# Kernel tuning notes

Measured on AMD Instinct MI355X. Metric: run time of the kernel, lower is better.

## Reference

```python
import jax, jax.numpy as jnp
import numpy as np


def _layernorm(x, g, b, eps=1e-5):
    m = x.mean(-1, keepdims=True)
    v = ((x - m) ** 2).mean(-1, keepdims=True)
    return (x - m) * jax.lax.rsqrt(v + eps) * g + b


def _silu(x):
    return x * jax.nn.sigmoid(x)


def _mamba_mixer(x, in_w, conv_w, conv_b, xp_w, dt_w, dt_b, A_log, Dp, out_w):
    # x: (B, L, C) ; HF Mamba slow-path math
    B, L, C = x.shape
    dI = in_w.shape[0] // 2
    h, gate = jnp.split(x @ in_w.T, 2, axis=-1)  # (B, L, dI) each
    hc = jnp.transpose(h, (0, 2, 1))             # (B, dI, L)
    K = conv_w.shape[-1]
    hc = jax.lax.conv_general_dilated(hc, conv_w, (1,), [(K - 1, 0)],
                                      feature_group_count=dI,
                                      dimension_numbers=('NCH', 'OIH', 'NCH'))
    hc = _silu(hc + conv_b[None, :, None])
    u = jnp.transpose(hc, (0, 2, 1))             # (B, L, dI)
    R = dt_w.shape[1]
    N = A_log.shape[1]
    dt, Bs, Cs = jnp.split(u @ xp_w.T, [R, R + N], axis=-1)
    dt = jax.nn.softplus(dt @ dt_w.T + dt_b)     # (B, L, dI)
    A = -jnp.exp(A_log)                          # (dI, N)
    dA = jnp.exp(dt[..., None] * A)              # (B, L, dI, N)
    dBu = dt[..., None] * Bs[:, :, None, :] * u[..., None]  # (B, L, dI, N)

    def step(state, inp):
        dA_t, dBu_t, C_t = inp
        state = dA_t * state + dBu_t             # (B, dI, N)
        y = jnp.einsum('bdn,bn->bd', state, C_t)
        return state, y

    h0 = jnp.zeros((B, dI, N), x.dtype)
    _, ys = jax.lax.scan(step, h0, (jnp.swapaxes(dA, 0, 1),
                                    jnp.swapaxes(dBu, 0, 1),
                                    jnp.swapaxes(Cs, 0, 1)))
    y = jnp.swapaxes(ys, 0, 1)                   # (B, L, dI)
    y = (y + u * Dp) * _silu(gate)
    return y @ out_w.T


def _mixffn(x, H, W, fc1_w, fc1_b, pe_w, pe_b, fc2_w, fc2_b):
    B, L, C = x.shape
    img = jnp.transpose(x, (0, 2, 1)).reshape(B, C, H, W)
    t = jnp.einsum('bchw,fc->bfhw', img, fc1_w[:, :, 0, 0]) + fc1_b[None, :, None, None]
    Fch = pe_w.shape[0]
    t = jax.lax.conv_general_dilated(t, pe_w, (1, 1), [(1, 1), (1, 1)],
                                     feature_group_count=Fch,
                                     dimension_numbers=('NCHW', 'OIHW', 'NCHW'))
    t = t + pe_b[None, :, None, None]
    t = jax.nn.gelu(t, approximate=False)
    t = jnp.einsum('bfhw,cf->bchw', t, fc2_w[:, :, 0, 0]) + fc2_b[None, :, None, None]
    return jnp.transpose(t.reshape(B, C, L), (0, 2, 1))


def _forward(x, norm1_g, norm1_b, in_w, conv_w, conv_b, xp_w, dt_w, dt_b, A_log, Dp,
             out_w, norm2_g, norm2_b, gate_w, fc1_w, fc1_b, pe_w, pe_b, fc2_w, fc2_b,
             rand_index, H, W):
    identity = x
    B = x.shape[0]
    x_in = jnp.concatenate([x, jnp.flip(x, 1), x[:, rand_index]], axis=0)  # (3B, L, C)
    xn = _layernorm(x_in, norm1_g, norm1_b)
    y = _mamba_mixer(xn, in_w, conv_w, conv_b, xp_w, dt_w, dt_b, A_log, Dp, out_w)
    fwd, rev, shf = jnp.split(y, 3, axis=0)
    rev = jnp.flip(rev, 1)
    inv = jnp.argsort(rand_index)
    shf = shf[:, inv]
    g_in = jnp.concatenate([fwd.mean(1), rev.mean(1), shf.mean(1)], axis=-1)  # (B, 3C)
    g = jax.nn.softmax(g_in @ gate_w.T, axis=-1)                              # (B, 3)
    y = g[:, 0, None, None] * fwd + g[:, 1, None, None] * rev + g[:, 2, None, None] * shf
    x1 = identity + y
    xn2 = _layernorm(x1, norm2_g, norm2_b)
    return x1 + _mixffn(xn2, H, W, fc1_w, fc1_b, pe_w, pe_b, fc2_w, fc2_b)


def setup_inputs() -> dict:
    B, H, W, C = 2, 64, 64, 128
    L = H * W
    dI, N, K, R, Fch = 384, 4, 4, 128, 512
    key = jax.random.key(0)
    ks = jax.random.split(key, 32)
    s = lambda i, shape, sc=0.02: jax.random.normal(ks[i], shape, jnp.float32) * sc
    A_log = jnp.log(jnp.broadcast_to(jnp.arange(1, N + 1, dtype=jnp.float32), (dI, N)))
    return {
        'x': jax.random.normal(ks[0], (B, L, C), jnp.float32),
        'rand_index': jax.random.permutation(ks[1], L),
        'H': H, 'W': W,
        'norm1_g': jnp.ones((C,), jnp.float32),
        'norm1_b': jnp.zeros((C,), jnp.float32),
        'in_w': s(2, (2 * dI, C)),
        'conv_w': s(3, (dI, 1, K), 0.1),
        'conv_b': jnp.zeros((dI,), jnp.float32),
        'xp_w': s(4, (R + 2 * N, dI)),
        'dt_w': s(5, (dI, R)),
        'dt_b': s(6, (dI,), 0.1),
        'A_log': A_log,
        'Dp': jnp.ones((dI,), jnp.float32),
        'out_w': s(7, (C, dI)),
        'norm2_g': jnp.ones((C,), jnp.float32),
        'norm2_b': jnp.zeros((C,), jnp.float32),
        'gate_w': s(8, (3, 3 * C)),
        'fc1_w': s(9, (Fch, C, 1, 1)),
        'fc1_b': jnp.zeros((Fch,), jnp.float32),
        'pe_w': s(10, (Fch, 1, 3, 3), 0.1),
        'pe_b': jnp.zeros((Fch,), jnp.float32),
        'fc2_w': s(11, (C, Fch, 1, 1)),
        'fc2_b': jnp.zeros((C,), jnp.float32),
    }


def reference(x, rand_index, H, W, norm1_g, norm1_b, in_w, conv_w, conv_b, xp_w,
              dt_w, dt_b, A_log, Dp, out_w, norm2_g, norm2_b, gate_w,
              fc1_w, fc1_b, pe_w, pe_b, fc2_w, fc2_b):
    return _forward(x, norm1_g, norm1_b, in_w, conv_w, conv_b, xp_w, dt_w, dt_b,
                    A_log, Dp, out_w, norm2_g, norm2_b, gate_w, fc1_w, fc1_b,
                    pe_w, pe_b, fc2_w, fc2_b, rand_index, H, W)
```

## Files before the change

### kernel.cpp

```cpp
#include <hip/hip_runtime.h>
#include <math.h>

#define LLEN 4096
#define CCH 128
#define DI 384
#define NST 4
#define SBN 6
#define NB 2
#define FCH 512
#define NCHUNK 128
#define TSTEP 32

typedef short bf16x8 __attribute__((ext_vector_type(8)));
typedef short bf16x4 __attribute__((ext_vector_type(4)));
typedef float f32x4 __attribute__((ext_vector_type(4)));
typedef float f32x8 __attribute__((ext_vector_type(8)));

__device__ __forceinline__ float wave_sum(float v) {
#pragma unroll
    for (int o = 32; o > 0; o >>= 1) v += __shfl_xor(v, o);
    return v;
}

__device__ __forceinline__ short f2bf(float f) {
    unsigned int u = __float_as_uint(f);
    unsigned int r = (u + 0x7fffu + ((u >> 16) & 1u)) >> 16;
    return (short)r;
}
__device__ __forceinline__ float bf2f(short s) {
    return __uint_as_float(((unsigned int)(unsigned short)s) << 16);
}

#define OFF_IN  0
#define OFF_DTC 98304
#define OFF_BC  245760
#define OFF_OUT 248832
#define OFF_FC1 297984
#define OFF_FC2 363520
#define OFF_END 429056
#define NCONV   281600
#define NCBLK   1100
#define GWCBLK  14
#define LN1OFF  (NCBLK + 576 + GWCBLK + 16)
#define LN1BLK  2048

__global__ __launch_bounds__(256) void conv_comp(const float* __restrict__ in_w,
                                                 const float* __restrict__ xp_w,
                                                 const float* __restrict__ dt_w,
                                                 const float* __restrict__ out_w,
                                                 const float* __restrict__ fc1_w,
                                                 const float* __restrict__ fc2_w,
                                                 const float* __restrict__ gate_w,
                                                 const int* __restrict__ ridx,
                                                 const float* __restrict__ x,
                                                 const float* __restrict__ n1g,
                                                 const float* __restrict__ n1b,
                                                 short* __restrict__ wb,
                                                 float* __restrict__ colsum,
                                                 float* __restrict__ gwc,
                                                 int* __restrict__ inv,
                                                 short* __restrict__ xn)
{
    int bid = blockIdx.x;
    if (bid < NCBLK) {
        int i = bid * 256 + threadIdx.x;
        if (i >= NCONV) return;
        int idx = (i < OFF_DTC) ? i : i + (OFF_OUT - OFF_DTC);
        float v;
        if (idx < OFF_DTC)      v = in_w[idx];
        else if (idx < OFF_OUT) v = xp_w[128 * 384 + (idx - OFF_BC)];
        else if (idx < OFF_FC1) v = out_w[idx - OFF_OUT];
        else if (idx < OFF_FC2) v = fc1_w[idx - OFF_FC1];
        else                    v = fc2_w[idx - OFF_FC2];
        wb[idx] = f2bf(v);
    } else if (bid < NCBLK + 576) {
        if (bid == NCBLK) {
            for (int i = threadIdx.x; i < SBN * DI; i += 256) colsum[i] = 0.f;
        }
        int ji = (bid - NCBLK) * 256 + threadIdx.x;
        int j = ji / 384, k = ji % 384;
        float acc = 0.f;
#pragma unroll 8
        for (int n = 0; n < 128; n++)
            acc += dt_w[j * 128 + n] * xp_w[n * 384 + k];
        wb[OFF_DTC + j * 384 + k] = f2bf(acc);
    } else if (bid < NCBLK + 576 + GWCBLK) {
        int idx = (bid - NCBLK - 576) * 256 + threadIdx.x;
        if (idx >= 3456) return;
        int j = idx / 1152, rem = idx % 1152;
        int s = rem / 384, d = rem % 384;
        float acc = 0.f;
#pragma unroll 8
        for (int c = 0; c < 128; c++)
            acc += gate_w[j * 384 + s * 128 + c] * out_w[c * 384 + d];
        gwc[idx] = acc;
    } else if (bid < LN1OFF) {
        int l = (bid - NCBLK - 576 - GWCBLK) * 256 + threadIdx.x;
        if (l < LLEN) inv[ridx[l]] = l;
    } else {
        int r = (bid - LN1OFF) * 4 + (threadIdx.x >> 6);
        int lane = threadIdx.x & 63;
        const float* src = x + (size_t)r * CCH;
        float v0 = src[lane], v1 = src[lane + 64];
        float m = wave_sum(v0 + v1) * (1.f / 128.f);
        float d0 = v0 - m, d1 = v1 - m;
        float var = wave_sum(d0 * d0 + d1 * d1) * (1.f / 128.f);
        float rstd = rsqrtf(var + 1e-5f);
        short* dst = xn + (size_t)r * CCH;
        dst[lane]      = f2bf(d0 * rstd * n1g[lane]      + n1b[lane]);
        dst[lane + 64] = f2bf(d1 * rstd * n1g[lane + 64] + n1b[lane + 64]);
    }
}

template<int EPI>
__global__ __launch_bounds__(256) void gemm_w(const short* __restrict__ A, int lda,
                                              const short* __restrict__ W, int ldw, int Ntot,
                                              const float* __restrict__ bias,
                                              const float* __restrict__ res, int ldr,
                                              float* __restrict__ C0,
                                              short* __restrict__ Cb, int ldc,
                                              float* __restrict__ extra,
                                              int Kd)
{
    __shared__ short Als[64 * 72];
    __shared__ short Wls[128 * 72];
    int tid = threadIdx.x;
    int wid = tid >> 6, lane = tid & 63;
    int wm = wid >> 1, wn = wid & 1;
    int l15 = lane & 15, l4 = lane >> 4;
    int bm = blockIdx.x * 64, bn = blockIdx.y * 128;
    int srow = tid >> 3, scol = (tid & 7) * 8;
    const bool tail = (EPI == 7) && (bn >= 384);
    f32x4 acc[2][4] = {};
    for (int k0 = 0; k0 < Kd; k0 += 64) {
        bf16x8 av0 = *(const bf16x8*)&A[(size_t)(bm + srow) * lda + k0 + scol];
        bf16x8 av1 = *(const bf16x8*)&A[(size_t)(bm + srow + 32) * lda + k0 + scol];
        bf16x8 wv[4];
#pragma unroll
        for (int q = 0; q < 4; q++) {
            if (EPI == 7) {
                wv[q] = bf16x8{};
                if (bn + srow + 32 * q < Ntot)
                    wv[q] = *(const bf16x8*)&W[(size_t)(bn + srow + 32 * q) * ldw + k0 + scol];
            } else {
                wv[q] = *(const bf16x8*)&W[(size_t)(bn + srow + 32 * q) * ldw + k0 + scol];
            }
        }
        __syncthreads();
        *(bf16x8*)&Als[srow * 72 + scol] = av0;
        *(bf16x8*)&Als[(srow + 32) * 72 + scol] = av1;
#pragma unroll
        for (int q = 0; q < 4; q++)
            *(bf16x8*)&Wls[(srow + 32 * q) * 72 + scol] = wv[q];
        __syncthreads();
        if (!tail) {
#pragma unroll
            for (int ks = 0; ks < 2; ks++) {
                bf16x8 af[2], bw[4];
#pragma unroll
                for (int f = 0; f < 2; f++)
                    af[f] = *(const bf16x8*)&Als[(wm * 32 + f * 16 + l15) * 72 + ks * 32 + l4 * 8];
#pragma unroll
                for (int j = 0; j < 4; j++)
                    bw[j] = *(const bf16x8*)&Wls[(wn * 64 + j * 16 + l15) * 72 + ks * 32 + l4 * 8];
#pragma unroll
                for (int i = 0; i < 2; i++)
#pragma unroll
                    for (int j = 0; j < 4; j++)
                        acc[i][j] = __builtin_amdgcn_mfma_f32_16x16x32_bf16(af[i], bw[j], acc[i][j], 0, 0, 0);
            }
        } else if (wn == 0) {
#pragma unroll
            for (int ks = 0; ks < 2; ks++) {
                bf16x8 af[2];
#pragma unroll
                for (int f = 0; f < 2; f++)
                    af[f] = *(const bf16x8*)&Als[(wm * 32 + f * 16 + l15) * 72 + ks * 32 + l4 * 8];
                bf16x8 bw0 = *(const bf16x8*)&Wls[(l15)*72 + ks * 32 + l4 * 8];
#pragma unroll
                for (int i = 0; i < 2; i++)
                    acc[i][0] = __builtin_amdgcn_mfma_f32_16x16x32_bf16(af[i], bw0, acc[i][0], 0, 0, 0);
            }
        }
    }
#pragma unroll
    for (int i = 0; i < 2; i++) {
        int row0 = bm + wm * 32 + i * 16 + l4 * 4;
#pragma unroll
        for (int j = 0; j < 4; j++) {
            int col = bn + wn * 64 + j * 16 + l15;
            if (EPI == 7) {
                if (col < 384) {
                    float bv = bias[col];
#pragma unroll
                    for (int r = 0; r < 4; r++) {
                        float v = acc[i][j][r] + bv;
                        v = (v > 20.f) ? v : __logf(1.f + __expf(v));
                        Cb[(size_t)(row0 + r) * ldc + col] = f2bf(v);
                    }
                } else if (col < 392) {
#pragma unroll
                    for (int r = 0; r < 4; r++)
                        extra[(size_t)(row0 + r) * 8 + (col - 384)] = acc[i][j][r];
                }
            } else {
                float bv = (EPI == 3 || EPI == 6) ? bias[col] : 0.f;
#pragma unroll
                for (int r = 0; r < 4; r++) {
                    float v = acc[i][j][r] + bv;
                    if (EPI == 3) v += res[(size_t)(row0 + r) * ldr + col];
                    if (EPI == 5 || EPI == 6)
                        Cb[(size_t)(row0 + r) * ldc + col] = f2bf(v);
                    else
                        C0[(size_t)(row0 + r) * ldc + col] = v;
                }
            }
        }
    }
}

__global__ __launch_bounds__(192) void dwconv_silu_v3(const short* __restrict__ hg,
                                                      const int* __restrict__ ridx,
                                                      const float* __restrict__ cw,
                                                      const float* __restrict__ cb,
                                                      short* __restrict__ ub)
{
    int t = threadIdx.x;
    int c = t % 48, rs = t / 48;
    int blk = blockIdx.x;
    int sb = blk >> 7;
    int s = sb >> 1, bb = sb & 1;
    int l0 = ((blk & 127) << 5) + rs * 8;
    int d0 = c * 8;
    float w0[8], w1[8], w2[8], w3[8], bs[8];
#pragma unroll
    for (int e = 0; e < 8; e++) {
        int d = d0 + e;
        bs[e] = cb[d];
        w0[e] = cw[d * 4 + 0]; w1[e] = cw[d * 4 + 1];
        w2[e] = cw[d * 4 + 2]; w3[e] = cw[d * 4 + 3];
    }
    float r0[8], r1[8], r2[8];
#pragma unroll
    for (int e = 0; e < 8; e++) { r0[e] = 0.f; r1[e] = 0.f; r2[e] = 0.f; }
    if (l0 - 3 >= 0) {
        int j = l0 - 3;
        int sl = (s == 0) ? j : (s == 1 ? LLEN - 1 - j : ridx[j]);
        bf16x8 v = *(const bf16x8*)&hg[(size_t)(bb * LLEN + sl) * 768 + d0];
#pragma unroll
        for (int e = 0; e < 8; e++) r0[e] = bf2f(v[e]);
    }
    if (l0 - 2 >= 0) {
        int j = l0 - 2;
        int sl = (s == 0) ? j : (s == 1 ? LLEN - 1 - j : ridx[j]);
        bf16x8 v = *(const bf16x8*)&hg[(size_t)(bb * LLEN + sl) * 768 + d0];
#pragma unroll
        for (int e = 0; e < 8; e++) r1[e] = bf2f(v[e]);
    }
    if (l0 - 1 >= 0) {
        int j = l0 - 1;
        int sl = (s == 0) ? j : (s == 1 ? LLEN - 1 - j : ridx[j]);
        bf16x8 v = *(const bf16x8*)&hg[(size_t)(bb * LLEN + sl) * 768 + d0];
#pragma unroll
        for (int e = 0; e < 8; e++) r2[e] = bf2f(v[e]);
    }
#pragma unroll
    for (int i = 0; i < 8; i++) {
        int j = l0 + i;
        int sl = (s == 0) ? j : (s == 1 ? LLEN - 1 - j : ridx[j]);
        bf16x8 v = *(const bf16x8*)&hg[(size_t)(bb * LLEN + sl) * 768 + d0];
        float r3[8];
#pragma unroll
        for (int e = 0; e < 8; e++) r3[e] = bf2f(v[e]);
        bf16x8 ov;
#pragma unroll
        for (int e = 0; e < 8; e++) {
            float a = bs[e] + w0[e] * r0[e] + w1[e] * r1[e] + w2[e] * r2[e] + w3[e] * r3[e];
            ov[e] = f2bf(a * __builtin_amdgcn_rcpf(1.f + __expf(-a)));
        }
        *(bf16x8*)&ub[(size_t)(sb * LLEN + j) * DI + d0] = ov;
#pragma unroll
        for (int e = 0; e < 8; e++) { r0[e] = r1[e]; r1[e] = r2[e]; r2[e] = r3[e]; }
    }
}

__global__ __launch_bounds__(DI) void scan_phaseA2(const short* __restrict__ dtb,
                                                   const float* __restrict__ bc,
                                                   const short* __restrict__ ub,
                                                   const float* __restrict__ A_log,
                                                   float* __restrict__ PS)
{
    __shared__ short ds_dt[TSTEP * DI];
    __shared__ short ds_u[TSTEP * DI];
    __shared__ float ds_bc[TSTEP * 8];
    int tid = threadIdx.x;
    int bid = blockIdx.x;
    int sb = bid / NCHUNK, chunk = bid % NCHUNK;
    int base = sb * LLEN + chunk * TSTEP;
    {
        int rr = tid / 48, cc = (tid % 48) * 8;
#pragma unroll
        for (int p = 0; p < 4; p++) {
            int row = p * 8 + rr;
            *(bf16x8*)&ds_dt[row * DI + cc] = *(const bf16x8*)&dtb[(size_t)(base + row) * DI + cc];
            *(bf16x8*)&ds_u[row * DI + cc]  = *(const bf16x8*)&ub[(size_t)(base + row) * DI + cc];
        }
        if (tid < TSTEP * 8) ds_bc[tid] = bc[(size_t)base * 8 + tid];
    }
    int d = tid;
    f32x4 al = *(const f32x4*)&A_log[d * 4];
    float a[NST];
#pragma unroll
    for (int n = 0; n < NST; n++) a[n] = -__expf(al[n]);
    __syncthreads();
    float s[NST] = {0.f, 0.f, 0.f, 0.f}, p[NST] = {1.f, 1.f, 1.f, 1.f};
    for (int t = 0; t < TSTEP; t++) {
        float dtv = bf2f(ds_dt[t * DI + d]);
        float dtu = dtv * bf2f(ds_u[t * DI + d]);
#pragma unroll
        for (int n = 0; n < NST; n++) {
            float dA = __expf(dtv * a[n]);
            s[n] = dA * s[n] + dtu * ds_bc[t * 8 + n];
            p[n] *= dA;
        }
    }
    f32x8 v;
#pragma unroll
    for (int n = 0; n < NST; n++) { v[2 * n] = p[n]; v[2 * n + 1] = s[n]; }
    *(f32x8*)&PS[(size_t)(sb * NCHUNK + chunk) * 3072 + d * 8] = v;
}

__global__ __launch_bounds__(256) void scan_phaseB2(const float* __restrict__ PS,
                                                    float* __restrict__ I)
{
    int gid = blockIdx.x * 256 + threadIdx.x;
    if (gid >= SBN * 1536) return;
    int sb = gid / 1536, dn = gid % 1536;
    const float* ps = PS + (size_t)sb * NCHUNK * 3072 + dn * 2;
    float* Ip = I + (size_t)sb * NCHUNK * 1536 + dn;
    float st = 0.f;
    for (int c = 0; c < NCHUNK; c += 8) {
        float2 v[8];
#pragma unroll
        for (int q = 0; q < 8; q++) v[q] = *(const float2*)&ps[(size_t)(c + q) * 3072];
#pragma unroll
        for (int q = 0; q < 8; q++) { Ip[(size_t)(c + q) * 1536] = st; st = v[q].x * st + v[q].y; }
    }
}

__global__ __launch_bounds__(DI) void scan_phaseC3(const short* __restrict__ dtb,
                                                   const float* __restrict__ bc,
                                                   const short* __restrict__ ub,
                                                   const short* __restrict__ hg,
                                                   const int* __restrict__ ridx,
                                                   const float* __restrict__ A_log,
                                                   const float* __restrict__ Dp,
                                                   const float* __restrict__ I,
                                                   short* __restrict__ ymix,
                                                   float* __restrict__ colsum)
{
    __shared__ short ds_dt[TSTEP * DI];
    __shared__ short ds_u[TSTEP * DI];
    __shared__ float ds_bc[TSTEP * 8];
    __shared__ int ds_src[TSTEP];
    int tid = threadIdx.x;
    int bid = blockIdx.x;
    int sb = bid / NCHUNK, chunk = bid % NCHUNK;
    int s2 = sb >> 1, bb = sb & 1;
    int base = sb * LLEN + chunk * TSTEP;
    {
        int rr = tid / 48, cc = (tid % 48) * 8;
#pragma unroll
        for (int p = 0; p < 4; p++) {
            int row = p * 8 + rr;
            *(bf16x8*)&ds_dt[row * DI + cc] = *(const bf16x8*)&dtb[(size_t)(base + row) * DI + cc];
            *(bf16x8*)&ds_u[row * DI + cc]  = *(const bf16x8*)&ub[(size_t)(base + row) * DI + cc];
        }
        if (tid < TSTEP * 8) ds_bc[tid] = bc[(size_t)base * 8 + tid];
        if (tid < TSTEP) {
            int l = chunk * TSTEP + tid;
            int sl = (s2 == 0) ? l : (s2 == 1 ? LLEN - 1 - l : ridx[l]);
            ds_src[tid] = bb * LLEN + sl;
        }
    }
    int d = tid;
    f32x4 al = *(const f32x4*)&A_log[d * 4];
    float a[NST];
#pragma unroll
    for (int n = 0; n < NST; n++) a[n] = -__expf(al[n]);
    __syncthreads();
    float s[NST];
    {
        f32x4 si = *(const f32x4*)&I[(size_t)(sb * NCHUNK + chunk) * 1536 + d * 4];
#pragma unroll
        for (int n = 0; n < NST; n++) s[n] = si[n];
    }
    float Dv = Dp[d];
    float csum = 0.f;
    for (int t = 0; t < TSTEP; t++) {
        float dtv = bf2f(ds_dt[t * DI + d]);
        float uv = bf2f(ds_u[t * DI + d]);
        float dtu = dtv * uv;
        float y = 0.f;
#pragma unroll
        for (int n = 0; n < NST; n++) {
            float dA = __expf(dtv * a[n]);
            s[n] = dA * s[n] + dtu * ds_bc[t * 8 + n];
            y += s[n] * ds_bc[t * 8 + 4 + n];
        }
        float gt = bf2f(hg[(size_t)ds_src[t] * 768 + 384 + d]);
        float sg = gt * __builtin_amdgcn_rcpf(1.f + __expf(-gt));
        float val = (y + uv * Dv) * sg;
        ymix[(size_t)(base + t) * DI + d] = f2bf(val);
        csum += val;
    }
    atomicAdd(&colsum[sb * DI + d], csum);
}

__global__ __launch_bounds__(256) void combine_outproj_ln2(const short* __restrict__ ymix,
                                                           const float* __restrict__ x,
                                                           const float* __restrict__ colsum,
                                                           const float* __restrict__ gwc,
                                                           const int* __restrict__ inv,
                                                           const short* __restrict__ Wout,
                                                           const float* __restrict__ n2g,
                                                           const float* __restrict__ n2b,
                                                           float* __restrict__ x1,
                                                           short* __restrict__ xn2)
{
    __shared__ short Als[64 * 72];
    __shared__ short Wls[128 * 72];
    __shared__ float xs[64][132];
    __shared__ int ssrc[192];
    __shared__ float msh[64], rsh[64];
    __shared__ float part[4][3];
    __shared__ float gsh[3];
    int tid = threadIdx.x;
    int bm = blockIdx.x * 64;
    int bb = bm >> 12;
    if (tid < 64) {
        int l = (bm & 4095) + tid;
        ssrc[tid * 3 + 0] = bb * LLEN + l;
        ssrc[tid * 3 + 1] = (2 + bb) * LLEN + (LLEN - 1 - l);
        ssrc[tid * 3 + 2] = (4 + bb) * LLEN + inv[l];
    }
    int wid = tid >> 6, lane = tid & 63;
    {
        float a0 = 0.f, a1 = 0.f, a2 = 0.f;
        for (int i = tid; i < 1152; i += 256) {
            int s = i / 384, d = i % 384;
            float cv = colsum[(s * 2 + bb) * 384 + d];
            a0 += cv * gwc[i];
            a1 += cv * gwc[1152 + i];
            a2 += cv * gwc[2304 + i];
        }
        a0 = wave_sum(a0); a1 = wave_sum(a1); a2 = wave_sum(a2);
        if (lane == 0) { part[wid][0] = a0; part[wid][1] = a1; part[wid][2] = a2; }
    }
    __syncthreads();
    if (tid == 0) {
        float l0 = 0.f, l1 = 0.f, l2 = 0.f;
#pragma unroll
        for (int w = 0; w < 4; w++) { l0 += part[w][0]; l1 += part[w][1]; l2 += part[w][2]; }
        l0 *= (1.f / 4096.f); l1 *= (1.f / 4096.f); l2 *= (1.f / 4096.f);
        float mx = fmaxf(l0, fmaxf(l1, l2));
        float e0 = __expf(l0 - mx), e1 = __expf(l1 - mx), e2 = __expf(l2 - mx);
        float iv = __builtin_amdgcn_rcpf(e0 + e1 + e2);
        gsh[0] = e0 * iv; gsh[1] = e1 * iv; gsh[2] = e2 * iv;
    }
    __syncthreads();
    float g0 = gsh[0], g1 = gsh[1], g2 = gsh[2];
    int wm = wid >> 1, wn = wid & 1;
    int l15 = lane & 15, l4 = lane >> 4;
    int srow = tid >> 3, scol = (tid & 7) * 8;
    f32x4 acc[2][4] = {};
    for (int k0 = 0; k0 < DI; k0 += 64) {
        bf16x8 cmb[2];
#pragma unroll
        for (int hh = 0; hh < 2; hh++) {
            int r = srow + 32 * hh;
            bf16x8 vf = *(const bf16x8*)&ymix[(size_t)ssrc[r * 3 + 0] * DI + k0 + scol];
            bf16x8 vr = *(const bf16x8*)&ymix[(size_t)ssrc[r * 3 + 1] * DI + k0 + scol];
            bf16x8 vs = *(const bf16x8*)&ymix[(size_t)ssrc[r * 3 + 2] * DI + k0 + scol];
#pragma unroll
            for (int e = 0; e < 8; e++)
                cmb[hh][e] = f2bf(g0 * bf2f(vf[e]) + g1 * bf2f(vr[e]) + g2 * bf2f(vs[e]));
        }
        bf16x8 wv[4];
#pragma unroll
        for (int q = 0; q < 4; q++)
            wv[q] = *(const bf16x8*)&Wout[(size_t)(srow + 32 * q) * DI + k0 + scol];
        __syncthreads();
        *(bf16x8*)&Als[srow * 72 + scol] = cmb[0];
        *(bf16x8*)&Als[(srow + 32) * 72 + scol] = cmb[1];
#pragma unroll
        for (int q = 0; q < 4; q++)
            *(bf16x8*)&Wls[(srow + 32 * q) * 72 + scol] = wv[q];
        __syncthreads();
#pragma unroll
        for (int ks = 0; ks < 2; ks++) {
            bf16x8 af[2], bw[4];
#pragma unroll
            for (int f = 0; f < 2; f++)
                af[f] = *(const bf16x8*)&Als[(wm * 32 + f * 16 + l15) * 72 + ks * 32 + l4 * 8];
#pragma unroll
            for (int j = 0; j < 4; j++)
                bw[j] = *(const bf16x8*)&Wls[(wn * 64 + j * 16 + l15) * 72 + ks * 32 + l4 * 8];
#pragma unroll
            for (int i = 0; i < 2; i++)
#pragma unroll
                for (int j = 0; j < 4; j++)
                    acc[i][j] = __builtin_amdgcn_mfma_f32_16x16x32_bf16(af[i], bw[j], acc[i][j], 0, 0, 0);
        }
    }
#pragma unroll
    for (int i = 0; i < 2; i++) {
        int rowl = wm * 32 + i * 16 + l4 * 4;
#pragma unroll
        for (int j = 0; j < 4; j++) {
            int col = wn * 64 + j * 16 + l15;
#pragma unroll
            for (int r = 0; r < 4; r++)
                xs[rowl + r][col] = acc[i][j][r] + x[(size_t)(bm + rowl + r) * CCH + col];
        }
    }
    __syncthreads();
    {
        int row = tid >> 2, q = tid & 3;
        float sum = 0.f, sq = 0.f;
#pragma unroll
        for (int c = q * 32; c < q * 32 + 32; c++) { float v = xs[row][c]; sum += v; sq += v * v; }
        sum += __shfl_xor(sum, 1); sq += __shfl_xor(sq, 1);
        sum += __shfl_xor(sum, 2); sq += __shfl_xor(sq, 2);
        if (q == 0) {
            float m = sum * (1.f / 128.f);
            float var = sq * (1.f / 128.f) - m * m;
            msh[row] = m;
            rsh[row] = rsqrtf(fmaxf(var, 0.f) + 1e-5f);
        }
    }
    __syncthreads();
    {
        int col = tid & 127;
        float gg = n2g[col], b2 = n2b[col];
#pragma unroll
        for (int e = 0; e < 32; e++) {
            int row = e * 2 + (tid >> 7);
            float v = xs[row][col];
            x1[(size_t)(bm + row) * CCH + col] = v;
            xn2[(size_t)(bm + row) * CCH + col] = f2bf((v - msh[row]) * rsh[row] * gg + b2);
        }
    }
}

__global__ __launch_bounds__(256) void peconv_gelu_v2(const short* __restrict__ t,
                                                      const float* __restrict__ pw,
                                                      const float* __restrict__ pb,
                                                      short* __restrict__ t2)
{
    int tid = threadIdx.x;
    int fc = tid & 127;
    int wsr = tid >> 7;
    int blk = blockIdx.x;
    int whalf = blk & 1, h = (blk >> 1) & 63, bb = blk >> 7;
    int w0 = whalf * 32 + wsr * 16;
    int f0 = fc * 4;
    float wt[9][4], bias4[4];
#pragma unroll
    for (int e = 0; e < 4; e++) {
        bias4[e] = pb[f0 + e];
#pragma unroll
        for (int k = 0; k < 9; k++) wt[k][e] = pw[(f0 + e) * 9 + k];
    }
    size_t base = (size_t)bb * 4096 * FCH;
    float cm1[3][4], cc[3][4], cn[3][4];
#pragma unroll
    for (int rr = 0; rr < 3; rr++)
#pragma unroll
        for (int e = 0; e < 4; e++) { cm1[rr][e] = 0.f; cc[rr][e] = 0.f; }
#pragma unroll
    for (int rr = 0; rr < 3; rr++) {
        int hh = h + rr - 1;
        if (hh >= 0 && hh < 64) {
            if (w0 - 1 >= 0) {
                bf16x4 v = *(const bf16x4*)&t[base + ((size_t)hh * 64 + (w0 - 1)) * FCH + f0];
#pragma unroll
                for (int e = 0; e < 4; e++) cm1[rr][e] = bf2f(v[e]);
            }
            bf16x4 v = *(const bf16x4*)&t[base + ((size_t)hh * 64 + w0) * FCH + f0];
#pragma unroll
            for (int e = 0; e < 4; e++) cc[rr][e] = bf2f(v[e]);
        }
    }
#pragma unroll
    for (int i = 0; i < 16; i++) {
        int w = w0 + i;
#pragma unroll
        for (int rr = 0; rr < 3; rr++) {
#pragma unroll
            for (int e = 0; e < 4; e++) cn[rr][e] = 0.f;
            int hh = h + rr - 1;
            if (hh >= 0 && hh < 64 && w + 1 < 64) {
                bf16x4 v = *(const bf16x4*)&t[base + ((size_t)hh * 64 + (w + 1)) * FCH + f0];
#pragma unroll
                for (int e = 0; e < 4; e++) cn[rr][e] = bf2f(v[e]);
            }
        }
        bf16x4 ov;
#pragma unroll
        for (int e = 0; e < 4; e++) {
            float acc = bias4[e];
#pragma unroll
            for (int rr = 0; rr < 3; rr++) {
                acc += wt[rr * 3 + 0][e] * cm1[rr][e];
                acc += wt[rr * 3 + 1][e] * cc[rr][e];
                acc += wt[rr * 3 + 2][e] * cn[rr][e];
            }
            ov[e] = f2bf(0.5f * acc * (1.f + erff(acc * 0.70710678118654752f)));
        }
        *(bf16x4*)&t2[base + ((size_t)h * 64 + w) * FCH + f0] = ov;
#pragma unroll
        for (int rr = 0; rr < 3; rr++)
#pragma unroll
            for (int e = 0; e < 4; e++) { cm1[rr][e] = cc[rr][e]; cc[rr][e] = cn[rr][e]; }
    }
}

extern "C" void kernel_launch(void* const* d_in, const int* in_sizes, int n_in,
                              void* d_out, int out_size, void* d_ws, size_t ws_size,
                              hipStream_t stream)
{
    (void)in_sizes; (void)n_in; (void)ws_size; (void)out_size;
    const float* x      = (const float*)d_in[0];
    const int*   ridx   = (const int*)d_in[1];
    const float* n1g    = (const float*)d_in[4];
    const float* n1b    = (const float*)d_in[5];
    const float* in_w   = (const float*)d_in[6];
    const float* conv_w = (const float*)d_in[7];
    const float* conv_b = (const float*)d_in[8];
    const float* xp_w   = (const float*)d_in[9];
    const float* dt_w   = (const float*)d_in[10];
    const float* dt_b   = (const float*)d_in[11];
    const float* A_log  = (const float*)d_in[12];
    const float* Dp     = (const float*)d_in[13];
    const float* out_w  = (const float*)d_in[14];
    const float* n2g    = (const float*)d_in[15];
    const float* n2b    = (const float*)d_in[16];
    const float* gate_w = (const float*)d_in[17];
    const float* fc1_w  = (const float*)d_in[18];
    const float* fc1_b  = (const float*)d_in[19];
    const float* pe_w   = (const float*)d_in[20];
    const float* pe_b   = (const float*)d_in[21];
    const float* fc2_w  = (const float*)d_in[22];
    const float* fc2_b  = (const float*)d_in[23];
    float* out = (float*)d_out;

    float* ws = (float*)d_ws;
    short* wb   = (short*)ws;
    float* regA = ws + 215040;
    float* regB = regA + 2097152;
    float* regC = regB + 9437184;
    float* regD = regC + 4718592;
    float* regE = regD + 4718592;
    float* regF = regE + 4718592;
    float* regG = regF + 2359296;
    float* smallb = regG + 196608;

    short* xn   = (short*)regA;
    float* Ibuf = regA;
    short* tbuf = (short*)regA;
    short* hg   = (short*)regB;
    float* x1   = regB + 3145728;
    short* xn2  = (short*)(regB + 4194304);
    short* t2   = (short*)(regB + 4718592);
    short* ub   = (short*)regC;
    short* ymix = (short*)regD;
    short* dtb  = (short*)regE;
    float* PS   = regF;
    float* xpbc = regG;
    float* colsum = smallb;
    float* gwcb   = smallb + 2304;
    float* gbuf   = gwcb + 3456;
    int*   invb   = (int*)(gbuf + 8);
    (void)gbuf;

    const int M6 = SBN * LLEN;
    const int M2 = NB * LLEN;

    conv_comp<<<LN1OFF + LN1BLK, 256, 0, stream>>>(in_w, xp_w, dt_w, out_w, fc1_w, fc2_w,
                                                   gate_w, ridx, x, n1g, n1b,
                                                   wb, colsum, gwcb, invb, xn);
    gemm_w<5><<<dim3(M2 / 64, 6), 256, 0, stream>>>(xn, CCH, wb + OFF_IN, CCH, 768, nullptr, nullptr, 0, nullptr, hg, 768, nullptr, CCH);
    dwconv_silu_v3<<<768, 192, 0, stream>>>(hg, ridx, conv_w, conv_b, ub);
    gemm_w<7><<<dim3(M6 / 64, 4), 256, 0, stream>>>(ub, DI, wb + OFF_DTC, DI, 392, dt_b, nullptr, 0, nullptr, dtb, DI, xpbc, DI);
    scan_phaseA2<<<SBN * NCHUNK, DI, 0, stream>>>(dtb, xpbc, ub, A_log, PS);
    scan_phaseB2<<<36, 256, 0, stream>>>(PS, Ibuf);
    scan_phaseC3<<<SBN * NCHUNK, DI, 0, stream>>>(dtb, xpbc, ub, hg, ridx, A_log, Dp, Ibuf, ymix, colsum);
    combine_outproj_ln2<<<M2 / 64, 256, 0, stream>>>(ymix, x, colsum, gwcb, invb, wb + OFF_OUT, n2g, n2b, x1, xn2);
    gemm_w<6><<<dim3(M2 / 64, 4), 256, 0, stream>>>(xn2, CCH, wb + OFF_FC1, CCH, FCH, fc1_b, nullptr, 0, nullptr, tbuf, FCH, nullptr, CCH);
    peconv_gelu_v2<<<256, 256, 0, stream>>>(tbuf, pe_w, pe_b, t2);
    gemm_w<3><<<dim3(M2 / 64, 1), 256, 0, stream>>>(t2, FCH, wb + OFF_FC2, FCH, CCH, fc2_b, x1, CCH, out, nullptr, CCH, nullptr, FCH);
}
```

Baseline: 173.6 us.

## Fuse B/C projection into dwconv, dedicated dt GEMM, fuse pe-conv with fc2

Computes the 8 B/C projection columns inside the depthwise conv+SiLU kernel using per-block shared-memory atomic reductions, so they are no longer part of the dt GEMM tail. The dt GEMM becomes a dedicated kernel that processes the full 384-wide output per block and reuses each A tile across all N columns. The positional depthwise conv+GELU output is kept in LDS and fed directly into the fc2 MFMA GEMM with the residual add, which removes the t2 global round trip and one launch. The cost is more LDS atomics, more register pressure, and larger LDS footprints that may lower occupancy.

```diff
diff --git a/kernel.cpp b/kernel.cpp
--- a/kernel.cpp
+++ b/kernel.cpp
@@ -114,12 +114,9 @@
 
 template<int EPI>
 __global__ __launch_bounds__(256) void gemm_w(const short* __restrict__ A, int lda,
-                                              const short* __restrict__ W, int ldw, int Ntot,
+                                              const short* __restrict__ W, int ldw,
                                               const float* __restrict__ bias,
-                                              const float* __restrict__ res, int ldr,
-                                              float* __restrict__ C0,
                                               short* __restrict__ Cb, int ldc,
-                                              float* __restrict__ extra,
                                               int Kd)
 {
     __shared__ short Als[64 * 72];
@@ -130,22 +127,14 @@
     int l15 = lane & 15, l4 = lane >> 4;
     int bm = blockIdx.x * 64, bn = blockIdx.y * 128;
     int srow = tid >> 3, scol = (tid & 7) * 8;
-    const bool tail = (EPI == 7) && (bn >= 384);
     f32x4 acc[2][4] = {};
     for (int k0 = 0; k0 < Kd; k0 += 64) {
         bf16x8 av0 = *(const bf16x8*)&A[(size_t)(bm + srow) * lda + k0 + scol];
         bf16x8 av1 = *(const bf16x8*)&A[(size_t)(bm + srow + 32) * lda + k0 + scol];
         bf16x8 wv[4];
 #pragma unroll
-        for (int q = 0; q < 4; q++) {
-            if (EPI == 7) {
-                wv[q] = bf16x8{};
-                if (bn + srow + 32 * q < Ntot)
-                    wv[q] = *(const bf16x8*)&W[(size_t)(bn + srow + 32 * q) * ldw + k0 + scol];
-            } else {
-                wv[q] = *(const bf16x8*)&W[(size_t)(bn + srow + 32 * q) * ldw + k0 + scol];
-            }
-        }
+        for (int q = 0; q < 4; q++)
+            wv[q] = *(const bf16x8*)&W[(size_t)(bn + srow + 32 * q) * ldw + k0 + scol];
         __syncthreads();
         *(bf16x8*)&Als[srow * 72 + scol] = av0;
         *(bf16x8*)&Als[(srow + 32) * 72 + scol] = av1;
@@ -153,34 +142,20 @@
         for (int q = 0; q < 4; q++)
             *(bf16x8*)&Wls[(srow + 32 * q) * 72 + scol] = wv[q];
         __syncthreads();
-        if (!tail) {
-#pragma unroll
-            for (int ks = 0; ks < 2; ks++) {
-                bf16x8 af[2], bw[4];
-#pragma unroll
-                for (int f = 0; f < 2; f++)
-                    af[f] = *(const bf16x8*)&Als[(wm * 32 + f * 16 + l15) * 72 + ks * 32 + l4 * 8];
+#pragma unroll
+        for (int ks = 0; ks < 2; ks++) {
+            bf16x8 af[2], bw[4];
+#pragma unroll
+            for (int f = 0; f < 2; f++)
+                af[f] = *(const bf16x8*)&Als[(wm * 32 + f * 16 + l15) * 72 + ks * 32 + l4 * 8];
+#pragma unroll
+            for (int j = 0; j < 4; j++)
+                bw[j] = *(const bf16x8*)&Wls[(wn * 64 + j * 16 + l15) * 72 + ks * 32 + l4 * 8];
+#pragma unroll
+            for (int i = 0; i < 2; i++)
 #pragma unroll
                 for (int j = 0; j < 4; j++)
-                    bw[j] = *(const bf16x8*)&Wls[(wn * 64 + j * 16 + l15) * 72 + ks * 32 + l4 * 8];
-#pragma unroll
-                for (int i = 0; i < 2; i++)
-#pragma unroll
-                    for (int j = 0; j < 4; j++)
-                        acc[i][j] = __builtin_amdgcn_mfma_f32_16x16x32_bf16(af[i], bw[j], acc[i][j], 0, 0, 0);
-            }
-        } else if (wn == 0) {
-#pragma unroll
-            for (int ks = 0; ks < 2; ks++) {
-                bf16x8 af[2];
-#pragma unroll
-                for (int f = 0; f < 2; f++)
-                    af[f] = *(const bf16x8*)&Als[(wm * 32 + f * 16 + l15) * 72 + ks * 32 + l4 * 8];
-                bf16x8 bw0 = *(const bf16x8*)&Wls[(l15)*72 + ks * 32 + l4 * 8];
-#pragma unroll
-                for (int i = 0; i < 2; i++)
-                    acc[i][0] = __builtin_amdgcn_mfma_f32_16x16x32_bf16(af[i], bw0, acc[i][0], 0, 0, 0);
-            }
+                    acc[i][j] = __builtin_amdgcn_mfma_f32_16x16x32_bf16(af[i], bw[j], acc[i][j], 0, 0, 0);
         }
     }
 #pragma unroll
@@ -189,43 +164,86 @@
 #pragma unroll
         for (int j = 0; j < 4; j++) {
             int col = bn + wn * 64 + j * 16 + l15;
-            if (EPI == 7) {
-                if (col < 384) {
-                    float bv = bias[col];
-#pragma unroll
-                    for (int r = 0; r < 4; r++) {
-                        float v = acc[i][j][r] + bv;
-                        v = (v > 20.f) ? v : __logf(1.f + __expf(v));
-                        Cb[(size_t)(row0 + r) * ldc + col] = f2bf(v);
-                    }
-                } else if (col < 392) {
-#pragma unroll
-                    for (int r = 0; r < 4; r++)
-                        extra[(size_t)(row0 + r) * 8 + (col - 384)] = acc[i][j][r];
-                }
-            } else {
-                float bv = (EPI == 3 || EPI == 6) ? bias[col] : 0.f;
-#pragma unroll
-                for (int r = 0; r < 4; r++) {
-                    float v = acc[i][j][r] + bv;
-                    if (EPI == 3) v += res[(size_t)(row0 + r) * ldr + col];
-                    if (EPI == 5 || EPI == 6)
-                        Cb[(size_t)(row0 + r) * ldc + col] = f2bf(v);
-                    else
-                        C0[(size_t)(row0 + r) * ldc + col] = v;
-                }
+            float bv = (EPI == 6) ? bias[col] : 0.f;
+#pragma unroll
+            for (int r = 0; r < 4; r++)
+                Cb[(size_t)(row0 + r) * ldc + col] = f2bf(acc[i][j][r] + bv);
+        }
+    }
+}
+
+__global__ __launch_bounds__(256) void gemm_dt(const short* __restrict__ A,
+                                               const short* __restrict__ W,
+                                               const float* __restrict__ bias,
+                                               short* __restrict__ Cb)
+{
+    __shared__ short Als[64 * 72];
+    __shared__ short Wls[384 * 72];
+    int tid = threadIdx.x;
+    int wid = tid >> 6, lane = tid & 63;
+    int wm = wid >> 1, wn = wid & 1;
+    int l15 = lane & 15, l4 = lane >> 4;
+    int bm = blockIdx.x * 64;
+    int srow = tid >> 3, scol = (tid & 7) * 8;
+    f32x4 acc[2][12] = {};
+    for (int k0 = 0; k0 < 384; k0 += 64) {
+        bf16x8 av0 = *(const bf16x8*)&A[(size_t)(bm + srow) * DI + k0 + scol];
+        bf16x8 av1 = *(const bf16x8*)&A[(size_t)(bm + srow + 32) * DI + k0 + scol];
+        bf16x8 wv[12];
+#pragma unroll
+        for (int q = 0; q < 12; q++)
+            wv[q] = *(const bf16x8*)&W[(size_t)(srow + 32 * q) * DI + k0 + scol];
+        __syncthreads();
+        *(bf16x8*)&Als[srow * 72 + scol] = av0;
+        *(bf16x8*)&Als[(srow + 32) * 72 + scol] = av1;
+#pragma unroll
+        for (int q = 0; q < 12; q++)
+            *(bf16x8*)&Wls[(srow + 32 * q) * 72 + scol] = wv[q];
+        __syncthreads();
+#pragma unroll
+        for (int ks = 0; ks < 2; ks++) {
+            bf16x8 af[2];
+#pragma unroll
+            for (int f = 0; f < 2; f++)
+                af[f] = *(const bf16x8*)&Als[(wm * 32 + f * 16 + l15) * 72 + ks * 32 + l4 * 8];
+#pragma unroll
+            for (int j = 0; j < 12; j++) {
+                bf16x8 bw = *(const bf16x8*)&Wls[(wn * 192 + j * 16 + l15) * 72 + ks * 32 + l4 * 8];
+#pragma unroll
+                for (int i = 0; i < 2; i++)
+                    acc[i][j] = __builtin_amdgcn_mfma_f32_16x16x32_bf16(af[i], bw, acc[i][j], 0, 0, 0);
             }
         }
     }
-}
-
-__global__ __launch_bounds__(192) void dwconv_silu_v3(const short* __restrict__ hg,
+#pragma unroll
+    for (int i = 0; i < 2; i++) {
+        int row0 = bm + wm * 32 + i * 16 + l4 * 4;
+#pragma unroll
+        for (int j = 0; j < 12; j++) {
+            int col = wn * 192 + j * 16 + l15;
+            float bv = bias[col];
+#pragma unroll
+            for (int r = 0; r < 4; r++) {
+                float v = acc[i][j][r] + bv;
+                v = (v > 20.f) ? v : __logf(1.f + __expf(v));
+                Cb[(size_t)(row0 + r) * DI + col] = f2bf(v);
+            }
+        }
+    }
+}
+
+__global__ __launch_bounds__(192) void dwconv_silu_v4(const short* __restrict__ hg,
                                                       const int* __restrict__ ridx,
                                                       const float* __restrict__ cw,
                                                       const float* __restrict__ cb,
-                                                      short* __restrict__ ub)
-{
+                                                      const float* __restrict__ xp_w,
+                                                      short* __restrict__ ub,
+                                                      float* __restrict__ xpbc)
+{
+    __shared__ float red[256];
     int t = threadIdx.x;
+    for (int i = t; i < 256; i += 192) red[i] = 0.f;
+    __syncthreads();
     int c = t % 48, rs = t / 48;
     int blk = blockIdx.x;
     int sb = blk >> 7;
@@ -240,6 +258,12 @@
         w0[e] = cw[d * 4 + 0]; w1[e] = cw[d * 4 + 1];
         w2[e] = cw[d * 4 + 2]; w3[e] = cw[d * 4 + 3];
     }
+    float xw[8][8];
+#pragma unroll
+    for (int n = 0; n < 8; n++)
+#pragma unroll
+        for (int e = 0; e < 8; e++)
+            xw[n][e] = xp_w[(size_t)(128 + n) * 384 + d0 + e];
     float r0[8], r1[8], r2[8];
 #pragma unroll
     for (int e = 0; e < 8; e++) { r0[e] = 0.f; r1[e] = 0.f; r2[e] = 0.f; }
@@ -269,19 +293,33 @@
         int j = l0 + i;
         int sl = (s == 0) ? j : (s == 1 ? LLEN - 1 - j : ridx[j]);
         bf16x8 v = *(const bf16x8*)&hg[(size_t)(bb * LLEN + sl) * 768 + d0];
-        float r3[8];
+        float r3[8], rf[8];
 #pragma unroll
         for (int e = 0; e < 8; e++) r3[e] = bf2f(v[e]);
         bf16x8 ov;
 #pragma unroll
         for (int e = 0; e < 8; e++) {
             float a = bs[e] + w0[e] * r0[e] + w1[e] * r1[e] + w2[e] * r2[e] + w3[e] * r3[e];
-            ov[e] = f2bf(a * __builtin_amdgcn_rcpf(1.f + __expf(-a)));
+            float r = a * __builtin_amdgcn_rcpf(1.f + __expf(-a));
+            rf[e] = r;
+            ov[e] = f2bf(r);
         }
         *(bf16x8*)&ub[(size_t)(sb * LLEN + j) * DI + d0] = ov;
+        int rib = rs * 8 + i;
+#pragma unroll
+        for (int n = 0; n < 8; n++) {
+            float p = 0.f;
+#pragma unroll
+            for (int e = 0; e < 8; e++) p += rf[e] * xw[n][e];
+            atomicAdd(&red[rib * 8 + n], p);
+        }
 #pragma unroll
         for (int e = 0; e < 8; e++) { r0[e] = r1[e]; r1[e] = r2[e]; r2[e] = r3[e]; }
     }
+    __syncthreads();
+    int rowbase = sb * LLEN + ((blk & 127) << 5);
+    for (int idx = t; idx < 256; idx += 192)
+        xpbc[(size_t)(rowbase + (idx >> 3)) * 8 + (idx & 7)] = red[idx];
 }
 
 __global__ __launch_bounds__(DI) void scan_phaseA2(const short* __restrict__ dtb,
@@ -553,11 +591,16 @@
     }
 }
 
-__global__ __launch_bounds__(256) void peconv_gelu_v2(const short* __restrict__ t,
-                                                      const float* __restrict__ pw,
-                                                      const float* __restrict__ pb,
-                                                      short* __restrict__ t2)
-{
+__global__ __launch_bounds__(256) void peconv_fc2(const short* __restrict__ t,
+                                                  const float* __restrict__ pw,
+                                                  const float* __restrict__ pb,
+                                                  const short* __restrict__ W2,
+                                                  const float* __restrict__ fc2_b,
+                                                  const float* __restrict__ x1,
+                                                  float* __restrict__ out)
+{
+    __shared__ short t2ls[32 * 520];
+    __shared__ short Wls[128 * 72];
     int tid = threadIdx.x;
     int fc = tid & 127;
     int wsr = tid >> 7;
@@ -565,64 +608,104 @@
     int whalf = blk & 1, h = (blk >> 1) & 63, bb = blk >> 7;
     int w0 = whalf * 32 + wsr * 16;
     int f0 = fc * 4;
-    float wt[9][4], bias4[4];
-#pragma unroll
-    for (int e = 0; e < 4; e++) {
-        bias4[e] = pb[f0 + e];
-#pragma unroll
-        for (int k = 0; k < 9; k++) wt[k][e] = pw[(f0 + e) * 9 + k];
-    }
-    size_t base = (size_t)bb * 4096 * FCH;
-    float cm1[3][4], cc[3][4], cn[3][4];
-#pragma unroll
-    for (int rr = 0; rr < 3; rr++)
-#pragma unroll
-        for (int e = 0; e < 4; e++) { cm1[rr][e] = 0.f; cc[rr][e] = 0.f; }
-#pragma unroll
-    for (int rr = 0; rr < 3; rr++) {
-        int hh = h + rr - 1;
-        if (hh >= 0 && hh < 64) {
-            if (w0 - 1 >= 0) {
-                bf16x4 v = *(const bf16x4*)&t[base + ((size_t)hh * 64 + (w0 - 1)) * FCH + f0];
-#pragma unroll
-                for (int e = 0; e < 4; e++) cm1[rr][e] = bf2f(v[e]);
+    {
+        float wt[9][4], bias4[4];
+#pragma unroll
+        for (int e = 0; e < 4; e++) {
+            bias4[e] = pb[f0 + e];
+#pragma unroll
+            for (int k = 0; k < 9; k++) wt[k][e] = pw[(f0 + e) * 9 + k];
+        }
+        size_t base = (size_t)bb * 4096 * FCH;
+        float cm1[3][4], cc[3][4], cn[3][4];
+#pragma unroll
+        for (int rr = 0; rr < 3; rr++)
+#pragma unroll
+            for (int e = 0; e < 4; e++) { cm1[rr][e] = 0.f; cc[rr][e] = 0.f; }
+#pragma unroll
+        for (int rr = 0; rr < 3; rr++) {
+            int hh = h + rr - 1;
+            if (hh >= 0 && hh < 64) {
+                if (w0 - 1 >= 0) {
+                    bf16x4 v = *(const bf16x4*)&t[base + ((size_t)hh * 64 + (w0 - 1)) * FCH + f0];
+#pragma unroll
+                    for (int e = 0; e < 4; e++) cm1[rr][e] = bf2f(v[e]);
+                }
+                bf16x4 v = *(const bf16x4*)&t[base + ((size_t)hh * 64 + w0) * FCH + f0];
+#pragma unroll
+                for (int e = 0; e < 4; e++) cc[rr][e] = bf2f(v[e]);
             }
-            bf16x4 v = *(const bf16x4*)&t[base + ((size_t)hh * 64 + w0) * FCH + f0];
-#pragma unroll
-            for (int e = 0; e < 4; e++) cc[rr][e] = bf2f(v[e]);
-        }
-    }
-#pragma unroll
-    for (int i = 0; i < 16; i++) {
-        int w = w0 + i;
-#pragma unroll
-        for (int rr = 0; rr < 3; rr++) {
-#pragma unroll
-            for (int e = 0; e < 4; e++) cn[rr][e] = 0.f;
-            int hh = h + rr - 1;
-            if (hh >= 0 && hh < 64 && w + 1 < 64) {
-                bf16x4 v = *(const bf16x4*)&t[base + ((size_t)hh * 64 + (w + 1)) * FCH + f0];
-#pragma unroll
-                for (int e = 0; e < 4; e++) cn[rr][e] = bf2f(v[e]);
+        }
+#pragma unroll
+        for (int i = 0; i < 16; i++) {
+            int w = w0 + i;
+#pragma unroll
+            for (int rr = 0; rr < 3; rr++) {
+#pragma unroll
+                for (int e = 0; e < 4; e++) cn[rr][e] = 0.f;
+                int hh = h + rr - 1;
+                if (hh >= 0 && hh < 64 && w + 1 < 64) {
+                    bf16x4 v = *(const bf16x4*)&t[base + ((size_t)hh * 64 + (w + 1)) * FCH + f0];
+#pragma unroll
+                    for (int e = 0; e < 4; e++) cn[rr][e] = bf2f(v[e]);
+                }
             }
-        }
-        bf16x4 ov;
-#pragma unroll
-        for (int e = 0; e < 4; e++) {
-            float acc = bias4[e];
-#pragma unroll
-            for (int rr = 0; rr < 3; rr++) {
-                acc += wt[rr * 3 + 0][e] * cm1[rr][e];
-                acc += wt[rr * 3 + 1][e] * cc[rr][e];
-                acc += wt[rr * 3 + 2][e] * cn[rr][e];
+            bf16x4 ov;
+#pragma unroll
+            for (int e = 0; e < 4; e++) {
+                float acc = bias4[e];
+#pragma unroll
+                for (int rr = 0; rr < 3; rr++) {
+                    acc += wt[rr * 3 + 0][e] * cm1[rr][e];
+                    acc += wt[rr * 3 + 1][e] * cc[rr][e];
+                    acc += wt[rr * 3 + 2][e] * cn[rr][e];
+                }
+                ov[e] = f2bf(0.5f * acc * (1.f + erff(acc * 0.70710678118654752f)));
             }
-            ov[e] = f2bf(0.5f * acc * (1.f + erff(acc * 0.70710678118654752f)));
-        }
-        *(bf16x4*)&t2[base + ((size_t)h * 64 + w) * FCH + f0] = ov;
-#pragma unroll
-        for (int rr = 0; rr < 3; rr++)
-#pragma unroll
-            for (int e = 0; e < 4; e++) { cm1[rr][e] = cc[rr][e]; cc[rr][e] = cn[rr][e]; }
+            int pix = wsr * 16 + i;
+            *(bf16x4*)&t2ls[pix * 520 + f0] = ov;
+#pragma unroll
+            for (int rr = 0; rr < 3; rr++)
+#pragma unroll
+                for (int e = 0; e < 4; e++) { cm1[rr][e] = cc[rr][e]; cc[rr][e] = cn[rr][e]; }
+        }
+    }
+    __syncthreads();
+    int wid = tid >> 6, lane = tid & 63;
+    int wm = wid >> 1, wn = wid & 1;
+    int l15 = lane & 15, l4 = lane >> 4;
+    int srow = tid >> 3, scol = (tid & 7) * 8;
+    int bm = bb * 4096 + h * 64 + whalf * 32;
+    f32x4 acc[4] = {};
+    for (int k0 = 0; k0 < FCH; k0 += 64) {
+        bf16x8 wv[4];
+#pragma unroll
+        for (int q = 0; q < 4; q++)
+            wv[q] = *(const bf16x8*)&W2[(size_t)(srow + 32 * q) * FCH + k0 + scol];
+        __syncthreads();
+#pragma unroll
+        for (int q = 0; q < 4; q++)
+            *(bf16x8*)&Wls[(srow + 32 * q) * 72 + scol] = wv[q];
+        __syncthreads();
+#pragma unroll
+        for (int ks = 0; ks < 2; ks++) {
+            bf16x8 af = *(const bf16x8*)&t2ls[(wm * 16 + l15) * 520 + k0 + ks * 32 + l4 * 8];
+#pragma unroll
+            for (int j = 0; j < 4; j++) {
+                bf16x8 bw = *(const bf16x8*)&Wls[(wn * 64 + j * 16 + l15) * 72 + ks * 32 + l4 * 8];
+                acc[j] = __builtin_amdgcn_mfma_f32_16x16x32_bf16(af, bw, acc[j], 0, 0, 0);
+            }
+        }
+    }
+#pragma unroll
+    for (int j = 0; j < 4; j++) {
+        int col = wn * 64 + j * 16 + l15;
+        float bv = fc2_b[col];
+#pragma unroll
+        for (int r = 0; r < 4; r++) {
+            int row = bm + wm * 16 + l4 * 4 + r;
+            out[(size_t)row * CCH + col] = acc[j][r] + bv + x1[(size_t)row * CCH + col];
+        }
     }
 }
 
@@ -672,7 +755,6 @@
     short* hg   = (short*)regB;
     float* x1   = regB + 3145728;
     short* xn2  = (short*)(regB + 4194304);
-    short* t2   = (short*)(regB + 4718592);
     short* ub   = (short*)regC;
     short* ymix = (short*)regD;
     short* dtb  = (short*)regE;
@@ -690,14 +772,13 @@
     conv_comp<<<LN1OFF + LN1BLK, 256, 0, stream>>>(in_w, xp_w, dt_w, out_w, fc1_w, fc2_w,
                                                    gate_w, ridx, x, n1g, n1b,
                                                    wb, colsum, gwcb, invb, xn);
-    gemm_w<5><<<dim3(M2 / 64, 6), 256, 0, stream>>>(xn, CCH, wb + OFF_IN, CCH, 768, nullptr, nullptr, 0, nullptr, hg, 768, nullptr, CCH);
-    dwconv_silu_v3<<<768, 192, 0, stream>>>(hg, ridx, conv_w, conv_b, ub);
-    gemm_w<7><<<dim3(M6 / 64, 4), 256, 0, stream>>>(ub, DI, wb + OFF_DTC, DI, 392, dt_b, nullptr, 0, nullptr, dtb, DI, xpbc, DI);
+    gemm_w<5><<<dim3(M2 / 64, 6), 256, 0, stream>>>(xn, CCH, wb + OFF_IN, CCH, nullptr, hg, 768, CCH);
+    dwconv_silu_v4<<<768, 192, 0, stream>>>(hg, ridx, conv_w, conv_b, xp_w, ub, xpbc);
+    gemm_dt<<<M6 / 64, 256, 0, stream>>>(ub, wb + OFF_DTC, dt_b, dtb);
     scan_phaseA2<<<SBN * NCHUNK, DI, 0, stream>>>(dtb, xpbc, ub, A_log, PS);
     scan_phaseB2<<<36, 256, 0, stream>>>(PS, Ibuf);
     scan_phaseC3<<<SBN * NCHUNK, DI, 0, stream>>>(dtb, xpbc, ub, hg, ridx, A_log, Dp, Ibuf, ymix, colsum);
     combine_outproj_ln2<<<M2 / 64, 256, 0, stream>>>(ymix, x, colsum, gwcb, invb, wb + OFF_OUT, n2g, n2b, x1, xn2);
-    gemm_w<6><<<dim3(M2 / 64, 4), 256, 0, stream>>>(xn2, CCH, wb + OFF_FC1, CCH, FCH, fc1_b, nullptr, 0, nullptr, tbuf, FCH, nullptr, CCH);
-    peconv_gelu_v2<<<256, 256, 0, stream>>>(tbuf, pe_w, pe_b, t2);
-    gemm_w<3><<<dim3(M2 / 64, 1), 256, 0, stream>>>(t2, FCH, wb + OFF_FC2, FCH, CCH, fc2_b, x1, CCH, out, nullptr, CCH, nullptr, FCH);
-}
+    gemm_w<6><<<dim3(M2 / 64, 4), 256, 0, stream>>>(xn2, CCH, wb + OFF_FC1, CCH, fc1_b, tbuf, FCH, CCH);
+    peconv_fc2<<<256, 256, 0, stream>>>(tbuf, pe_w, pe_b, wb + OFF_FC2, fc2_b, x1, out);
+}
```

After: 222.6 us. +28.2%, slower.
